# Kernel optimization log

Hardware: AMD Instinct MI355X
Metric: run time of the kernel (lower is better)

The kernel has to match this reference:

```python
import jax, jax.numpy as jnp
import numpy as np

B, HW, FEAT = 64, 196, 2048
EMB, HID, ATT, VOCAB, T = 512, 1024, 512, 10000, 20
STEPS = T - 1  # pack_padded_sequence uses lengths - 1


def setup_inputs() -> dict:
    key = jax.random.key(0)
    ks = jax.random.split(key, 16)
    rn = lambda k, s, sc=0.02: jax.random.normal(k, s, jnp.float32) * sc
    return {
        "features": jax.random.normal(ks[0], (B, HW, FEAT), jnp.float32),
        "captions": jax.random.randint(ks[1], (B, T), 0, VOCAB),
        "lengths": jnp.full((B,), T, jnp.int32),  # uniform lengths -> constant batch per step
        "E": rn(ks[2], (VOCAB, EMB)),
        "W_feat": rn(ks[3], (EMB, FEAT)), "b_feat": jnp.zeros((EMB,), jnp.float32),
        "W1": rn(ks[4], (ATT, EMB)), "b1": jnp.zeros((ATT,), jnp.float32),
        "W2": rn(ks[5], (ATT, HID)), "b2": jnp.zeros((ATT,), jnp.float32),
        "V": rn(ks[6], (1, ATT)), "bV": jnp.zeros((1,), jnp.float32),
        "W_hi": rn(ks[7], (HID, EMB)), "b_hi": jnp.zeros((HID,), jnp.float32),
        "W_ci": rn(ks[8], (HID, EMB)), "b_ci": jnp.zeros((HID,), jnp.float32),
        "W_ih": rn(ks[9], (4 * HID, 2 * EMB)), "b_ih": jnp.zeros((4 * HID,), jnp.float32),
        "W_hh": rn(ks[10], (4 * HID, HID)), "b_hh": jnp.zeros((4 * HID,), jnp.float32),
        "W_out": rn(ks[11], (VOCAB, HID)), "b_out": jnp.zeros((VOCAB,), jnp.float32),
    }


def reference(features, captions, lengths, E, W_feat, b_feat, W1, b1, W2, b2,
              V, bV, W_hi, b_hi, W_ci, b_ci, W_ih, b_ih, W_hh, b_hh, W_out, b_out):
    # features -> embed space: [B, HW, EMB]
    f = jnp.einsum('bhc,ec->bhe', features, W_feat) + b_feat
    fmean = f.mean(axis=1)                      # [B, EMB]
    hx0 = fmean @ W_hi.T + b_hi                 # [B, HID]
    cx0 = fmean @ W_ci.T + b_ci                 # [B, HID]
    fa = jnp.einsum('bhe,ae->bha', f, W1) + b1  # W1(features), [B, HW, ATT]

    emb = E[captions]                           # [B, T, EMB]
    xs = jnp.swapaxes(emb[:, :STEPS], 0, 1)     # [STEPS, B, EMB] teacher-forced inputs

    def step(carry, x):
        hx, cx = carry
        # Bahdanau attention
        ha = hx @ W2.T + b2                             # [B, ATT]
        score = jnp.tanh(fa + ha[:, None, :])           # [B, HW, ATT]
        logits = jnp.einsum('bha,oa->bho', score, V) + bV   # [B, HW, 1]
        w = jax.nn.softmax(logits, axis=1)              # softmax over HW
        ctx = jnp.sum(w * f, axis=1)                    # [B, EMB]
        # LSTMCell (PyTorch gate order: i, f, g, o)
        inp = jnp.concatenate([x, ctx], axis=1)         # [B, 2*EMB]
        gates = inp @ W_ih.T + b_ih + hx @ W_hh.T + b_hh
        i_g, f_g, g_g, o_g = jnp.split(gates, 4, axis=1)
        cx_n = jax.nn.sigmoid(f_g) * cx + jax.nn.sigmoid(i_g) * jnp.tanh(g_g)
        hx_n = jax.nn.sigmoid(o_g) * jnp.tanh(cx_n)
        out = hx_n @ W_out.T + b_out                    # dropout = identity (eval)
        return (hx_n, cx_n), out

    _, outs = jax.lax.scan(step, (hx0, cx0), xs)        # [STEPS, B, VOCAB]
    # torch.cat(outputs) over constant per-step batch == flatten time-major
    return outs.reshape(STEPS * B, VOCAB)
```

## Files before the change

### kernel.cpp

```cpp
#include <hip/hip_runtime.h>
#include <hip/hip_bf16.h>
#include <math.h>

#define BB 64
#define HW 196
#define FEAT 2048
#define EMB 512
#define HID 1024
#define ATT 512
#define VOCAB 10000
#define TT 20
#define STEPS 19

using bfrag = __attribute__((ext_vector_type(8))) short;
using f32x4 = __attribute__((ext_vector_type(4))) float;

__device__ __forceinline__ float sigmoid_fast(float x) { return 1.0f / (1.0f + __expf(-x)); }
__device__ __forceinline__ float tanh_fast(float x) {
    float e = __expf(2.0f * x);
    return 1.0f - 2.0f / (e + 1.0f);
}
__device__ __forceinline__ ushort f2bf_rne(float f) {
    unsigned u = __float_as_uint(f);
    unsigned r = (u + 0x7FFFu + ((u >> 16) & 1u)) >> 16;
    return (ushort)r;
}
__device__ __forceinline__ float bf2f(ushort h) {
    return __uint_as_float(((unsigned)h) << 16);
}

__global__ __launch_bounds__(256) void k_split(const float* __restrict__ x,
                                               ushort* __restrict__ hi,
                                               ushort* __restrict__ lo, int n)
{
    int i4 = (blockIdx.x * 256 + threadIdx.x) * 4;
    if (i4 >= n) return;
    float4 v = *(const float4*)(x + i4);
    float av[4] = {v.x, v.y, v.z, v.w};
    #pragma unroll
    for (int j = 0; j < 4; ++j) {
        ushort h = f2bf_rne(av[j]);
        hi[i4 + j] = h;
        lo[i4 + j] = f2bf_rne(av[j] - bf2f(h));
    }
}

template<bool ABF32, bool NFAST>
__global__ __launch_bounds__(256) void mfma_g(
    const float* __restrict__ A,
    const ushort* __restrict__ Ahi, const ushort* __restrict__ Alo,
    const ushort* __restrict__ Bhi, const ushort* __restrict__ Blo,
    const float* __restrict__ bias, float* __restrict__ C,
    ushort* __restrict__ Chi, ushort* __restrict__ Clo,
    int N, int K, int ldc, int NXB, int NMB)
{
    __shared__ __align__(16) ushort sAh[4][64][8];
    __shared__ __align__(16) ushort sAl[4][64][8];
    __shared__ __align__(16) ushort sBh[4][128][8];
    __shared__ __align__(16) ushort sBl[4][128][8];

    const int tid = threadIdx.x;

    const int nwg = NXB * NMB;
    const int q = nwg >> 3, r = nwg & 7;
    const int xcd = blockIdx.x & 7, sidx = blockIdx.x >> 3;
    const int wg = (xcd < r) ? (xcd * (q + 1) + sidx)
                             : (r * (q + 1) + (xcd - r) * q + sidx);
    int im, inb;
    if (NFAST) { inb = wg % NXB; im = wg / NXB; }
    else       { im = wg % NMB; inb = wg / NMB; }
    const int m0 = im * 64;
    const int n0 = inb * 128;

    const int lane = tid & 63;
    const int w = tid >> 6;
    const int mh = (w & 1) * 32;
    const int nh = (w >> 1) * 64;
    const int g = lane >> 4, l15 = lane & 15;

    f32x4 acc[2][4] = {};

    for (int k0 = 0; k0 < K; k0 += 32) {
        __syncthreads();
        if (ABF32) {
            int r_ = tid >> 2, g_ = tid & 3;
            const float* ap = A + (size_t)(m0 + r_) * K + k0 + g_ * 8;
            float av[8];
            *(float4*)(av)     = *(const float4*)(ap);
            *(float4*)(av + 4) = *(const float4*)(ap + 4);
            bfrag vh, vl;
            #pragma unroll
            for (int j = 0; j < 8; ++j) {
                ushort h = f2bf_rne(av[j]);
                vh[j] = (short)h;
                vl[j] = (short)f2bf_rne(av[j] - bf2f(h));
            }
            *(bfrag*)&sAh[g_][r_][0] = vh;
            *(bfrag*)&sAl[g_][r_][0] = vl;
        } else {
            #pragma unroll
            for (int i = 0; i < 2; ++i) {
                int c = tid + i * 256;
                int pl = c >> 8, idx2 = c & 255;
                int r_ = idx2 >> 2, g_ = idx2 & 3;
                const ushort* src = (pl ? Alo : Ahi) + (size_t)(m0 + r_) * K + k0 + g_ * 8;
                if (pl) *(bfrag*)&sAl[g_][r_][0] = *(const bfrag*)src;
                else    *(bfrag*)&sAh[g_][r_][0] = *(const bfrag*)src;
            }
        }
        #pragma unroll
        for (int i = 0; i < 4; ++i) {
            int c = tid + i * 256;
            int pl = c >> 9, idx2 = c & 511;
            int r_ = idx2 >> 2, g_ = idx2 & 3;
            int brow = min(n0 + r_, N - 1);
            const ushort* src = (pl ? Blo : Bhi) + (size_t)brow * K + k0 + g_ * 8;
            if (pl) *(bfrag*)&sBl[g_][r_][0] = *(const bfrag*)src;
            else    *(bfrag*)&sBh[g_][r_][0] = *(const bfrag*)src;
        }
        __syncthreads();

        bfrag ah[2], al[2], bh[4], bl[4];
        #pragma unroll
        for (int s = 0; s < 2; ++s) {
            ah[s] = *(const bfrag*)&sAh[g][mh + s * 16 + l15][0];
            al[s] = *(const bfrag*)&sAl[g][mh + s * 16 + l15][0];
        }
        #pragma unroll
        for (int u = 0; u < 4; ++u) {
            bh[u] = *(const bfrag*)&sBh[g][nh + u * 16 + l15][0];
            bl[u] = *(const bfrag*)&sBl[g][nh + u * 16 + l15][0];
        }
        #pragma unroll
        for (int s = 0; s < 2; ++s)
            #pragma unroll
            for (int u = 0; u < 4; ++u) {
                acc[s][u] = __builtin_amdgcn_mfma_f32_16x16x32_bf16(ah[s], bh[u], acc[s][u], 0, 0, 0);
                acc[s][u] = __builtin_amdgcn_mfma_f32_16x16x32_bf16(ah[s], bl[u], acc[s][u], 0, 0, 0);
                acc[s][u] = __builtin_amdgcn_mfma_f32_16x16x32_bf16(al[s], bh[u], acc[s][u], 0, 0, 0);
            }
    }

    #pragma unroll
    for (int s = 0; s < 2; ++s)
        #pragma unroll
        for (int u = 0; u < 4; ++u) {
            int col = n0 + nh + u * 16 + l15;
            if (col < N) {
                float bv = bias[col];
                #pragma unroll
                for (int rr = 0; rr < 4; ++rr) {
                    int row = m0 + mh + s * 16 + g * 4 + rr;
                    float v = acc[s][u][rr] + bv;
                    C[(size_t)row * ldc + col] = v;
                    if (Chi) {
                        ushort hh = f2bf_rne(v);
                        Chi[(size_t)row * ldc + col] = hh;
                        Clo[(size_t)row * ldc + col] = f2bf_rne(v - bf2f(hh));
                    }
                }
            }
        }
}

__global__ __launch_bounds__(256) void k_fmean(const float* __restrict__ f,
                                               float* __restrict__ fmean)
{
    int b = blockIdx.x, tid = threadIdx.x;
    for (int e = tid; e < EMB; e += 256) {
        const float* fb = f + (size_t)b * HW * EMB + e;
        float s = 0.f;
        for (int h = 0; h < HW; ++h) s += fb[(size_t)h * EMB];
        fmean[b * EMB + e] = s * (1.0f / HW);
    }
}

__global__ __launch_bounds__(256) void k_init(
    const float* __restrict__ fmean,
    const float* __restrict__ W_hi, const float* __restrict__ b_hi,
    const float* __restrict__ W_ci, const float* __restrict__ b_ci,
    float* __restrict__ hx, float* __restrict__ cx)
{
    int b = blockIdx.x, tid = threadIdx.x;
    __shared__ float fm[EMB];
    for (int i = tid; i < EMB; i += 256) fm[i] = fmean[b * EMB + i];
    __syncthreads();
    for (int u = tid; u < HID; u += 256) {
        const float4* w1 = (const float4*)(W_hi + (size_t)u * EMB);
        const float4* w2 = (const float4*)(W_ci + (size_t)u * EMB);
        float a1 = b_hi[u], a2 = b_ci[u];
        for (int k = 0; k < EMB / 4; ++k) {
            float4 y1 = w1[k], y2 = w2[k];
            float x0 = fm[4*k], x1 = fm[4*k+1], x2 = fm[4*k+2], x3 = fm[4*k+3];
            a1 += x0*y1.x + x1*y1.y + x2*y1.z + x3*y1.w;
            a2 += x0*y2.x + x1*y2.y + x2*y2.z + x3*y2.w;
        }
        hx[b * HID + u] = a1;
        cx[b * HID + u] = a2;
    }
}

__global__ __launch_bounds__(128) void k_embed_split(
    const int* __restrict__ cap, const float* __restrict__ E,
    ushort* __restrict__ xs_hi, ushort* __restrict__ xs_lo)
{
    int blk = blockIdx.x;
    int t = blk / BB, b = blk % BB;
    int c = cap[b * TT + t];
    float4 v = ((const float4*)(E + (size_t)c * EMB))[threadIdx.x];
    float av[4] = {v.x, v.y, v.z, v.w};
    ushort h[4], l[4];
    #pragma unroll
    for (int j = 0; j < 4; ++j) {
        h[j] = f2bf_rne(av[j]);
        l[j] = f2bf_rne(av[j] - bf2f(h[j]));
    }
    size_t base = ((size_t)t * BB + b) * EMB + threadIdx.x * 4;
    *(ushort4*)(xs_hi + base) = make_ushort4(h[0], h[1], h[2], h[3]);
    *(ushort4*)(xs_lo + base) = make_ushort4(l[0], l[1], l[2], l[3]);
}

__global__ __launch_bounds__(256) void k_ha(
    const float* __restrict__ hx, const float* __restrict__ W2,
    const float* __restrict__ b2, float* __restrict__ ha)
{
    __shared__ __align__(16) float hx_s[8][1028];
    __shared__ float part[256];
    const int tid = threadIdx.x;
    const int a0 = (blockIdx.x >> 3) * 16;
    const int b0 = (blockIdx.x & 7) * 8;

    for (int i = tid; i < 8 * 256; i += 256) {
        int r = i >> 8, c4 = i & 255;
        *(float4*)&hx_s[r][c4 * 4] = *(const float4*)(hx + (size_t)(b0 + r) * HID + c4 * 4);
    }
    __syncthreads();

    const int a_i = tid >> 4;
    const int b_i = (tid >> 1) & 7;
    const int half = tid & 1;
    const float4* wr = (const float4*)(W2 + (size_t)(a0 + a_i) * HID + half * 512);
    const float* xr = &hx_s[b_i][half * 512];
    float s = 0.f;
    #pragma unroll 8
    for (int i = 0; i < 128; ++i) {
        float4 w = wr[i];
        float4 x = *(const float4*)(xr + i * 4);
        s += w.x*x.x + w.y*x.y + w.z*x.z + w.w*x.w;
    }
    part[tid] = s;
    __syncthreads();
    if (!half)
        ha[(size_t)(b0 + b_i) * ATT + a0 + a_i] = part[tid] + part[tid + 1] + b2[a0 + a_i];
}

__global__ __launch_bounds__(1024) void k_att(
    const float* __restrict__ f, const float* __restrict__ fa,
    const float* __restrict__ ha, const float* __restrict__ V,
    ushort* __restrict__ ctx_hi, ushort* __restrict__ ctx_lo)
{
    __shared__ __align__(16) float smem[2048];
    const int b = blockIdx.x;
    const int tid = threadIdx.x;
    const int lane = tid & 63;
    const int wid = tid >> 6;

    float* ha_s = smem;
    float* V_s  = smem + 512;
    float* w_s  = smem + 1024;
    float* red  = smem + 1280;
    float* pc   = smem + 1536;

    if (tid < ATT) { ha_s[tid] = ha[b * ATT + tid]; V_s[tid] = V[tid]; }
    __syncthreads();

    for (int h = wid; h < HW; h += 16) {
        const float4* fr = (const float4*)(fa + ((size_t)b * HW + h) * ATT);
        float s = 0.f;
        #pragma unroll
        for (int q = 0; q < 2; ++q) {
            int i4 = q * 64 + lane;
            float4 fv = fr[i4];
            float4 hv = *(const float4*)&ha_s[i4 * 4];
            float4 vv = *(const float4*)&V_s[i4 * 4];
            s += tanh_fast(fv.x + hv.x) * vv.x + tanh_fast(fv.y + hv.y) * vv.y
               + tanh_fast(fv.z + hv.z) * vv.z + tanh_fast(fv.w + hv.w) * vv.w;
        }
        #pragma unroll
        for (int off = 32; off > 0; off >>= 1) s += __shfl_down(s, off);
        if (lane == 0) w_s[h] = s;
    }
    __syncthreads();

    float v = (tid < HW) ? w_s[tid] : -INFINITY;
    if (tid < 256) red[tid] = v;
    __syncthreads();
    for (int s2 = 128; s2 > 0; s2 >>= 1) {
        if (tid < s2) red[tid] = fmaxf(red[tid], red[tid + s2]);
        __syncthreads();
    }
    float mx = red[0];
    __syncthreads();
    float e = (tid < HW) ? __expf(v - mx) : 0.f;
    if (tid < 256) red[tid] = e;
    __syncthreads();
    for (int s2 = 128; s2 > 0; s2 >>= 1) {
        if (tid < s2) red[tid] += red[tid + s2];
        __syncthreads();
    }
    float inv = 1.0f / red[0];
    if (tid < HW) w_s[tid] = e * inv;
    __syncthreads();

    {
        int e0 = tid & 511, grp = tid >> 9;
        const float* fb = f + (size_t)b * HW * EMB + e0;
        float s = 0.f;
        int h0 = grp * 98;
        for (int h = h0; h < h0 + 98; ++h)
            s = fmaf(w_s[h], fb[(size_t)h * EMB], s);
        if (grp) pc[e0] = s;
        __syncthreads();
        if (!grp) {
            float c = s + pc[e0];
            ushort ch = f2bf_rne(c);
            ctx_hi[b * EMB + e0] = ch;
            ctx_lo[b * EMB + e0] = f2bf_rne(c - bf2f(ch));
        }
    }
}

__global__ __launch_bounds__(256) void k_gates_lstm(
    const ushort* __restrict__ xsh, const ushort* __restrict__ xsl,
    const ushort* __restrict__ cth, const ushort* __restrict__ ctl,
    const ushort* __restrict__ hxh, const ushort* __restrict__ hxl,
    const ushort* __restrict__ wihh, const ushort* __restrict__ wihl,
    const ushort* __restrict__ whhh, const ushort* __restrict__ whhl,
    const float* __restrict__ b_ih, const float* __restrict__ b_hh,
    float* __restrict__ hx, float* __restrict__ cx,
    ushort* __restrict__ nxh, ushort* __restrict__ nxl,
    float* __restrict__ hx_all_t,
    ushort* __restrict__ hxa_h, ushort* __restrict__ hxa_l)
{
    __shared__ float sg[64][16];
    const int tid = threadIdx.x, bk = blockIdx.x;
    const int lane = tid & 63, mt = tid >> 6;
    const int l15 = lane & 15, g = lane >> 4;
    const int arow = mt * 16 + l15;
    const int ncol = (l15 >> 2) * 1024 + bk * 4 + (l15 & 3);
    const int koff = g * 8;

    f32x4 acc0 = {}, acc1 = {};

    {
        const ushort* ah = xsh + (size_t)arow * 512 + koff;
        const ushort* al = xsl + (size_t)arow * 512 + koff;
        const ushort* bh = wihh + (size_t)ncol * 1024 + koff;
        const ushort* bl = wihl + (size_t)ncol * 1024 + koff;
        #pragma unroll 4
        for (int kk = 0; kk < 16; ++kk) {
            bfrag a_h = *(const bfrag*)(ah + kk * 32);
            bfrag a_l = *(const bfrag*)(al + kk * 32);
            bfrag b_h = *(const bfrag*)(bh + kk * 32);
            bfrag b_l = *(const bfrag*)(bl + kk * 32);
            acc0 = __builtin_amdgcn_mfma_f32_16x16x32_bf16(a_h, b_h, acc0, 0, 0, 0);
            acc1 = __builtin_amdgcn_mfma_f32_16x16x32_bf16(a_h, b_l, acc1, 0, 0, 0);
            acc1 = __builtin_amdgcn_mfma_f32_16x16x32_bf16(a_l, b_h, acc1, 0, 0, 0);
        }
    }
    {
        const ushort* ah = cth + (size_t)arow * 512 + koff;
        const ushort* al = ctl + (size_t)arow * 512 + koff;
        const ushort* bh = wihh + (size_t)ncol * 1024 + 512 + koff;
        const ushort* bl = wihl + (size_t)ncol * 1024 + 512 + koff;
        #pragma unroll 4
        for (int kk = 0; kk < 16; ++kk) {
            bfrag a_h = *(const bfrag*)(ah + kk * 32);
            bfrag a_l = *(const bfrag*)(al + kk * 32);
            bfrag b_h = *(const bfrag*)(bh + kk * 32);
            bfrag b_l = *(const bfrag*)(bl + kk * 32);
            acc0 = __builtin_amdgcn_mfma_f32_16x16x32_bf16(a_h, b_h, acc0, 0, 0, 0);
            acc1 = __builtin_amdgcn_mfma_f32_16x16x32_bf16(a_h, b_l, acc1, 0, 0, 0);
            acc1 = __builtin_amdgcn_mfma_f32_16x16x32_bf16(a_l, b_h, acc1, 0, 0, 0);
        }
    }
    {
        const ushort* ah = hxh + (size_t)arow * 1024 + koff;
        const ushort* al = hxl + (size_t)arow * 1024 + koff;
        const ushort* bh = whhh + (size_t)ncol * 1024 + koff;
        const ushort* bl = whhl + (size_t)ncol * 1024 + koff;
        #pragma unroll 4
        for (int kk = 0; kk < 32; ++kk) {
            bfrag a_h = *(const bfrag*)(ah + kk * 32);
            bfrag a_l = *(const bfrag*)(al + kk * 32);
            bfrag b_h = *(const bfrag*)(bh + kk * 32);
            bfrag b_l = *(const bfrag*)(bl + kk * 32);
            acc0 = __builtin_amdgcn_mfma_f32_16x16x32_bf16(a_h, b_h, acc0, 0, 0, 0);
            acc1 = __builtin_amdgcn_mfma_f32_16x16x32_bf16(a_h, b_l, acc1, 0, 0, 0);
            acc1 = __builtin_amdgcn_mfma_f32_16x16x32_bf16(a_l, b_h, acc1, 0, 0, 0);
        }
    }

    #pragma unroll
    for (int rr = 0; rr < 4; ++rr)
        sg[mt * 16 + g * 4 + rr][l15] = acc0[rr] + acc1[rr];
    __syncthreads();

    {
        int b = tid >> 2, uu = tid & 3;
        int u = bk * 4 + uu;
        float gi = sg[b][uu]      + b_ih[u]        + b_hh[u];
        float gf = sg[b][4 + uu]  + b_ih[1024 + u] + b_hh[1024 + u];
        float gg = sg[b][8 + uu]  + b_ih[2048 + u] + b_hh[2048 + u];
        float go = sg[b][12 + uu] + b_ih[3072 + u] + b_hh[3072 + u];
        int idx = b * 1024 + u;
        float c = sigmoid_fast(gf) * cx[idx] + sigmoid_fast(gi) * tanh_fast(gg);
        float h = sigmoid_fast(go) * tanh_fast(c);
        cx[idx] = c;
        hx[idx] = h;
        hx_all_t[idx] = h;
        ushort hh = f2bf_rne(h);
        ushort hl = f2bf_rne(h - bf2f(hh));
        nxh[idx] = hh; nxl[idx] = hl;
        hxa_h[idx] = hh; hxa_l[idx] = hl;
    }
}

extern "C" void kernel_launch(void* const* d_in, const int* in_sizes, int n_in,
                              void* d_out, int out_size, void* d_ws, size_t ws_size,
                              hipStream_t stream) {
    const float* features = (const float*)d_in[0];
    const int*   captions = (const int*)d_in[1];
    const float* E      = (const float*)d_in[3];
    const float* W_feat = (const float*)d_in[4];
    const float* b_feat = (const float*)d_in[5];
    const float* W1     = (const float*)d_in[6];
    const float* b1     = (const float*)d_in[7];
    const float* W2     = (const float*)d_in[8];
    const float* b2     = (const float*)d_in[9];
    const float* V      = (const float*)d_in[10];
    const float* W_hi   = (const float*)d_in[12];
    const float* b_hi   = (const float*)d_in[13];
    const float* W_ci   = (const float*)d_in[14];
    const float* b_ci   = (const float*)d_in[15];
    const float* W_ih   = (const float*)d_in[16];
    const float* b_ih   = (const float*)d_in[17];
    const float* W_hh   = (const float*)d_in[18];
    const float* b_hh   = (const float*)d_in[19];
    const float* W_out  = (const float*)d_in[20];
    const float* b_out  = (const float*)d_in[21];
    float* out = (float*)d_out;

    float* ws = (float*)d_ws;
    float* f_buf   = ws;
    float* fa_buf  = f_buf + 6422528;
    float* fmean   = fa_buf + 6422528;
    float* hx      = fmean + 32768;
    float* cx      = hx + 65536;
    float* hx_all  = cx + 65536;
    float* ha      = hx_all + 1310720;
    ushort* p = (ushort*)(ha + 32768);
    ushort* f_hi     = p;            p += 6422528;
    ushort* f_lo     = p;            p += 6422528;
    ushort* wfeat_hi = p;            p += 1048576;
    ushort* wfeat_lo = p;            p += 1048576;
    ushort* w1_hi    = p;            p += 262144;
    ushort* w1_lo    = p;            p += 262144;
    ushort* wih_hi   = p;            p += 4194304;
    ushort* wih_lo   = p;            p += 4194304;
    ushort* whh_hi   = p;            p += 4194304;
    ushort* whh_lo   = p;            p += 4194304;
    ushort* xs_hi    = p;            p += 622592;
    ushort* xs_lo    = p;            p += 622592;
    ushort* ctx_hi   = p;            p += 32768;
    ushort* ctx_lo   = p;            p += 32768;
    ushort* hxp      = p;            p += 262144;
    ushort* hxa_hi   = p;            p += 1310720;
    ushort* hxa_lo   = p;            p += 1310720;
    ushort* wout_hi = (ushort*)f_buf;
    ushort* wout_lo = wout_hi + 10240000;

    k_split<<<1048576 / 4 / 256, 256, 0, stream>>>(W_feat, wfeat_hi, wfeat_lo, 1048576);
    k_split<<<262144 / 4 / 256, 256, 0, stream>>>(W1, w1_hi, w1_lo, 262144);
    k_split<<<4194304 / 4 / 256, 256, 0, stream>>>(W_ih, wih_hi, wih_lo, 4194304);
    k_split<<<4194304 / 4 / 256, 256, 0, stream>>>(W_hh, whh_hi, whh_lo, 4194304);
    mfma_g<true, true><<<784, 256, 0, stream>>>(
        features, nullptr, nullptr, wfeat_hi, wfeat_lo, b_feat,
        f_buf, f_hi, f_lo, 512, 2048, 512, 4, 196);
    mfma_g<false, true><<<784, 256, 0, stream>>>(
        nullptr, f_hi, f_lo, w1_hi, w1_lo, b1,
        fa_buf, nullptr, nullptr, 512, 512, 512, 4, 196);
    k_fmean<<<BB, 256, 0, stream>>>(f_buf, fmean);
    k_init<<<BB, 256, 0, stream>>>(fmean, W_hi, b_hi, W_ci, b_ci, hx, cx);
    k_split<<<65536 / 4 / 256, 256, 0, stream>>>(hx, hxp, hxp + 65536, 65536);
    k_embed_split<<<STEPS * BB, 128, 0, stream>>>(captions, E, xs_hi, xs_lo);

    for (int t = 0; t < STEPS; ++t) {
        ushort* hx_rd = hxp + (size_t)(t & 1) * 131072;
        ushort* hx_wr = hxp + (size_t)((t + 1) & 1) * 131072;
        k_ha<<<256, 256, 0, stream>>>(hx, W2, b2, ha);
        k_att<<<BB, 1024, 0, stream>>>(f_buf, fa_buf, ha, V, ctx_hi, ctx_lo);
        k_gates_lstm<<<256, 256, 0, stream>>>(
            xs_hi + (size_t)t * BB * EMB, xs_lo + (size_t)t * BB * EMB,
            ctx_hi, ctx_lo, hx_rd, hx_rd + 65536,
            wih_hi, wih_lo, whh_hi, whh_lo, b_ih, b_hh,
            hx, cx, hx_wr, hx_wr + 65536,
            hx_all + (size_t)t * BB * HID,
            hxa_hi + (size_t)t * BB * HID, hxa_lo + (size_t)t * BB * HID);
    }

    k_split<<<10240000 / 4 / 256, 256, 0, stream>>>(W_out, wout_hi, wout_lo, 10240000);
    mfma_g<false, false><<<1501, 256, 0, stream>>>(
        nullptr, hxa_hi, hxa_lo, wout_hi, wout_lo, b_out,
        out, nullptr, nullptr, VOCAB, HID, VOCAB, 79, 19);
}
```

Baseline: 1.887 ms.

## Swizzle LDS tiles, drop bf16 split buffers, split LSTM gate K across waves

The GEMM kernel now always reads fp32 A and splits it into hi/lo bf16 in-register, which removes the f_hi/f_lo and hxa_hi/hxa_lo intermediate buffers and their global writes. Shared-memory tiles use an XOR swizzle on the 16-byte chunk index to reduce LDS bank conflicts. The LSTM gate kernel doubles its threads so that the input-projection and recurrent-projection halves run on separate waves, with the partial sums combined through shared memory. The trade-off is re-splitting A inside every GEMM tile, which adds conversion ALU work and more fp32 read bandwidth.

Result: faster. 1.798 ms (-4.7%).

```diff
diff --git a/kernel.cpp b/kernel.cpp
--- a/kernel.cpp
+++ b/kernel.cpp
@@ -28,6 +28,7 @@
 __device__ __forceinline__ float bf2f(ushort h) {
     return __uint_as_float(((unsigned)h) << 16);
 }
+__device__ __forceinline__ int sw_idx(int row, int g) { return row * 4 + (g ^ (row & 3)); }
 
 __global__ __launch_bounds__(256) void k_split(const float* __restrict__ x,
                                                ushort* __restrict__ hi,
@@ -45,19 +46,17 @@
     }
 }
 
-template<bool ABF32, bool NFAST>
+template<bool NFAST>
 __global__ __launch_bounds__(256) void mfma_g(
     const float* __restrict__ A,
-    const ushort* __restrict__ Ahi, const ushort* __restrict__ Alo,
     const ushort* __restrict__ Bhi, const ushort* __restrict__ Blo,
     const float* __restrict__ bias, float* __restrict__ C,
-    ushort* __restrict__ Chi, ushort* __restrict__ Clo,
     int N, int K, int ldc, int NXB, int NMB)
 {
-    __shared__ __align__(16) ushort sAh[4][64][8];
-    __shared__ __align__(16) ushort sAl[4][64][8];
-    __shared__ __align__(16) ushort sBh[4][128][8];
-    __shared__ __align__(16) ushort sBl[4][128][8];
+    __shared__ __align__(16) ushort sAh[256 * 8];
+    __shared__ __align__(16) ushort sAl[256 * 8];
+    __shared__ __align__(16) ushort sBh[512 * 8];
+    __shared__ __align__(16) ushort sBl[512 * 8];
 
     const int tid = threadIdx.x;
 
@@ -82,7 +81,7 @@
 
     for (int k0 = 0; k0 < K; k0 += 32) {
         __syncthreads();
-        if (ABF32) {
+        {
             int r_ = tid >> 2, g_ = tid & 3;
             const float* ap = A + (size_t)(m0 + r_) * K + k0 + g_ * 8;
             float av[8];
@@ -95,18 +94,9 @@
                 vh[j] = (short)h;
                 vl[j] = (short)f2bf_rne(av[j] - bf2f(h));
             }
-            *(bfrag*)&sAh[g_][r_][0] = vh;
-            *(bfrag*)&sAl[g_][r_][0] = vl;
-        } else {
-            #pragma unroll
-            for (int i = 0; i < 2; ++i) {
-                int c = tid + i * 256;
-                int pl = c >> 8, idx2 = c & 255;
-                int r_ = idx2 >> 2, g_ = idx2 & 3;
-                const ushort* src = (pl ? Alo : Ahi) + (size_t)(m0 + r_) * K + k0 + g_ * 8;
-                if (pl) *(bfrag*)&sAl[g_][r_][0] = *(const bfrag*)src;
-                else    *(bfrag*)&sAh[g_][r_][0] = *(const bfrag*)src;
-            }
+            int c = sw_idx(r_, g_) * 8;
+            *(bfrag*)&sAh[c] = vh;
+            *(bfrag*)&sAl[c] = vl;
         }
         #pragma unroll
         for (int i = 0; i < 4; ++i) {
@@ -115,21 +105,24 @@
             int r_ = idx2 >> 2, g_ = idx2 & 3;
             int brow = min(n0 + r_, N - 1);
             const ushort* src = (pl ? Blo : Bhi) + (size_t)brow * K + k0 + g_ * 8;
-            if (pl) *(bfrag*)&sBl[g_][r_][0] = *(const bfrag*)src;
-            else    *(bfrag*)&sBh[g_][r_][0] = *(const bfrag*)src;
+            int cc = sw_idx(r_, g_) * 8;
+            if (pl) *(bfrag*)&sBl[cc] = *(const bfrag*)src;
+            else    *(bfrag*)&sBh[cc] = *(const bfrag*)src;
         }
         __syncthreads();
 
         bfrag ah[2], al[2], bh[4], bl[4];
         #pragma unroll
         for (int s = 0; s < 2; ++s) {
-            ah[s] = *(const bfrag*)&sAh[g][mh + s * 16 + l15][0];
-            al[s] = *(const bfrag*)&sAl[g][mh + s * 16 + l15][0];
+            int c = sw_idx(mh + s * 16 + l15, g) * 8;
+            ah[s] = *(const bfrag*)&sAh[c];
+            al[s] = *(const bfrag*)&sAl[c];
         }
         #pragma unroll
         for (int u = 0; u < 4; ++u) {
-            bh[u] = *(const bfrag*)&sBh[g][nh + u * 16 + l15][0];
-            bl[u] = *(const bfrag*)&sBl[g][nh + u * 16 + l15][0];
+            int c = sw_idx(nh + u * 16 + l15, g) * 8;
+            bh[u] = *(const bfrag*)&sBh[c];
+            bl[u] = *(const bfrag*)&sBl[c];
         }
         #pragma unroll
         for (int s = 0; s < 2; ++s)
@@ -151,13 +144,7 @@
                 #pragma unroll
                 for (int rr = 0; rr < 4; ++rr) {
                     int row = m0 + mh + s * 16 + g * 4 + rr;
-                    float v = acc[s][u][rr] + bv;
-                    C[(size_t)row * ldc + col] = v;
-                    if (Chi) {
-                        ushort hh = f2bf_rne(v);
-                        Chi[(size_t)row * ldc + col] = hh;
-                        Clo[(size_t)row * ldc + col] = f2bf_rne(v - bf2f(hh));
-                    }
+                    C[(size_t)row * ldc + col] = acc[s][u][rr] + bv;
                 }
             }
         }
@@ -330,7 +317,7 @@
     }
 }
 
-__global__ __launch_bounds__(256) void k_gates_lstm(
+__global__ __launch_bounds__(512) void k_gates_lstm(
     const ushort* __restrict__ xsh, const ushort* __restrict__ xsl,
     const ushort* __restrict__ cth, const ushort* __restrict__ ctl,
     const ushort* __restrict__ hxh, const ushort* __restrict__ hxl,
@@ -339,12 +326,12 @@
     const float* __restrict__ b_ih, const float* __restrict__ b_hh,
     float* __restrict__ hx, float* __restrict__ cx,
     ushort* __restrict__ nxh, ushort* __restrict__ nxl,
-    float* __restrict__ hx_all_t,
-    ushort* __restrict__ hxa_h, ushort* __restrict__ hxa_l)
-{
-    __shared__ float sg[64][16];
+    float* __restrict__ hx_all_t)
+{
+    __shared__ float sg[2][64][16];
     const int tid = threadIdx.x, bk = blockIdx.x;
-    const int lane = tid & 63, mt = tid >> 6;
+    const int lane = tid & 63, wid = tid >> 6;
+    const int mt = wid & 3, kh = wid >> 2;
     const int l15 = lane & 15, g = lane >> 4;
     const int arow = mt * 16 + l15;
     const int ncol = (l15 >> 2) * 1024 + bk * 4 + (l15 & 3);
@@ -352,39 +339,40 @@
 
     f32x4 acc0 = {}, acc1 = {};
 
-    {
-        const ushort* ah = xsh + (size_t)arow * 512 + koff;
-        const ushort* al = xsl + (size_t)arow * 512 + koff;
-        const ushort* bh = wihh + (size_t)ncol * 1024 + koff;
-        const ushort* bl = wihl + (size_t)ncol * 1024 + koff;
-        #pragma unroll 4
-        for (int kk = 0; kk < 16; ++kk) {
-            bfrag a_h = *(const bfrag*)(ah + kk * 32);
-            bfrag a_l = *(const bfrag*)(al + kk * 32);
-            bfrag b_h = *(const bfrag*)(bh + kk * 32);
-            bfrag b_l = *(const bfrag*)(bl + kk * 32);
-            acc0 = __builtin_amdgcn_mfma_f32_16x16x32_bf16(a_h, b_h, acc0, 0, 0, 0);
-            acc1 = __builtin_amdgcn_mfma_f32_16x16x32_bf16(a_h, b_l, acc1, 0, 0, 0);
-            acc1 = __builtin_amdgcn_mfma_f32_16x16x32_bf16(a_l, b_h, acc1, 0, 0, 0);
-        }
-    }
-    {
-        const ushort* ah = cth + (size_t)arow * 512 + koff;
-        const ushort* al = ctl + (size_t)arow * 512 + koff;
-        const ushort* bh = wihh + (size_t)ncol * 1024 + 512 + koff;
-        const ushort* bl = wihl + (size_t)ncol * 1024 + 512 + koff;
-        #pragma unroll 4
-        for (int kk = 0; kk < 16; ++kk) {
-            bfrag a_h = *(const bfrag*)(ah + kk * 32);
-            bfrag a_l = *(const bfrag*)(al + kk * 32);
-            bfrag b_h = *(const bfrag*)(bh + kk * 32);
-            bfrag b_l = *(const bfrag*)(bl + kk * 32);
-            acc0 = __builtin_amdgcn_mfma_f32_16x16x32_bf16(a_h, b_h, acc0, 0, 0, 0);
-            acc1 = __builtin_amdgcn_mfma_f32_16x16x32_bf16(a_h, b_l, acc1, 0, 0, 0);
-            acc1 = __builtin_amdgcn_mfma_f32_16x16x32_bf16(a_l, b_h, acc1, 0, 0, 0);
-        }
-    }
-    {
+    if (kh == 0) {
+        {
+            const ushort* ah = xsh + (size_t)arow * 512 + koff;
+            const ushort* al = xsl + (size_t)arow * 512 + koff;
+            const ushort* bh = wihh + (size_t)ncol * 1024 + koff;
+            const ushort* bl = wihl + (size_t)ncol * 1024 + koff;
+            #pragma unroll 4
+            for (int kk = 0; kk < 16; ++kk) {
+                bfrag a_h = *(const bfrag*)(ah + kk * 32);
+                bfrag a_l = *(const bfrag*)(al + kk * 32);
+                bfrag b_h = *(const bfrag*)(bh + kk * 32);
+                bfrag b_l = *(const bfrag*)(bl + kk * 32);
+                acc0 = __builtin_amdgcn_mfma_f32_16x16x32_bf16(a_h, b_h, acc0, 0, 0, 0);
+                acc1 = __builtin_amdgcn_mfma_f32_16x16x32_bf16(a_h, b_l, acc1, 0, 0, 0);
+                acc1 = __builtin_amdgcn_mfma_f32_16x16x32_bf16(a_l, b_h, acc1, 0, 0, 0);
+            }
+        }
+        {
+            const ushort* ah = cth + (size_t)arow * 512 + koff;
+            const ushort* al = ctl + (size_t)arow * 512 + koff;
+            const ushort* bh = wihh + (size_t)ncol * 1024 + 512 + koff;
+            const ushort* bl = wihl + (size_t)ncol * 1024 + 512 + koff;
+            #pragma unroll 4
+            for (int kk = 0; kk < 16; ++kk) {
+                bfrag a_h = *(const bfrag*)(ah + kk * 32);
+                bfrag a_l = *(const bfrag*)(al + kk * 32);
+                bfrag b_h = *(const bfrag*)(bh + kk * 32);
+                bfrag b_l = *(const bfrag*)(bl + kk * 32);
+                acc0 = __builtin_amdgcn_mfma_f32_16x16x32_bf16(a_h, b_h, acc0, 0, 0, 0);
+                acc1 = __builtin_amdgcn_mfma_f32_16x16x32_bf16(a_h, b_l, acc1, 0, 0, 0);
+                acc1 = __builtin_amdgcn_mfma_f32_16x16x32_bf16(a_l, b_h, acc1, 0, 0, 0);
+            }
+        }
+    } else {
         const ushort* ah = hxh + (size_t)arow * 1024 + koff;
         const ushort* al = hxl + (size_t)arow * 1024 + koff;
         const ushort* bh = whhh + (size_t)ncol * 1024 + koff;
@@ -403,16 +391,16 @@
 
     #pragma unroll
     for (int rr = 0; rr < 4; ++rr)
-        sg[mt * 16 + g * 4 + rr][l15] = acc0[rr] + acc1[rr];
-    __syncthreads();
-
-    {
+        sg[kh][mt * 16 + g * 4 + rr][l15] = acc0[rr] + acc1[rr];
+    __syncthreads();
+
+    if (tid < 256) {
         int b = tid >> 2, uu = tid & 3;
         int u = bk * 4 + uu;
-        float gi = sg[b][uu]      + b_ih[u]        + b_hh[u];
-        float gf = sg[b][4 + uu]  + b_ih[1024 + u] + b_hh[1024 + u];
-        float gg = sg[b][8 + uu]  + b_ih[2048 + u] + b_hh[2048 + u];
-        float go = sg[b][12 + uu] + b_ih[3072 + u] + b_hh[3072 + u];
+        float gi = sg[0][b][uu]      + sg[1][b][uu]      + b_ih[u]        + b_hh[u];
+        float gf = sg[0][b][4 + uu]  + sg[1][b][4 + uu]  + b_ih[1024 + u] + b_hh[1024 + u];
+        float gg = sg[0][b][8 + uu]  + sg[1][b][8 + uu]  + b_ih[2048 + u] + b_hh[2048 + u];
+        float go = sg[0][b][12 + uu] + sg[1][b][12 + uu] + b_ih[3072 + u] + b_hh[3072 + u];
         int idx = b * 1024 + u;
         float c = sigmoid_fast(gf) * cx[idx] + sigmoid_fast(gi) * tanh_fast(gg);
         float h = sigmoid_fast(go) * tanh_fast(c);
@@ -420,9 +408,8 @@
         hx[idx] = h;
         hx_all_t[idx] = h;
         ushort hh = f2bf_rne(h);
-        ushort hl = f2bf_rne(h - bf2f(hh));
-        nxh[idx] = hh; nxl[idx] = hl;
-        hxa_h[idx] = hh; hxa_l[idx] = hl;
+        nxh[idx] = hh;
+        nxl[idx] = f2bf_rne(h - bf2f(hh));
     }
 }
 
@@ -460,8 +447,6 @@
     float* hx_all  = cx + 65536;
     float* ha      = hx_all + 1310720;
     ushort* p = (ushort*)(ha + 32768);
-    ushort* f_hi     = p;            p += 6422528;
-    ushort* f_lo     = p;            p += 6422528;
     ushort* wfeat_hi = p;            p += 1048576;
     ushort* wfeat_lo = p;            p += 1048576;
     ushort* w1_hi    = p;            p += 262144;
@@ -475,8 +460,6 @@
     ushort* ctx_hi   = p;            p += 32768;
     ushort* ctx_lo   = p;            p += 32768;
     ushort* hxp      = p;            p += 262144;
-    ushort* hxa_hi   = p;            p += 1310720;
-    ushort* hxa_lo   = p;            p += 1310720;
     ushort* wout_hi = (ushort*)f_buf;
     ushort* wout_lo = wout_hi + 10240000;
 
@@ -484,12 +467,10 @@
     k_split<<<262144 / 4 / 256, 256, 0, stream>>>(W1, w1_hi, w1_lo, 262144);
     k_split<<<4194304 / 4 / 256, 256, 0, stream>>>(W_ih, wih_hi, wih_lo, 4194304);
     k_split<<<4194304 / 4 / 256, 256, 0, stream>>>(W_hh, whh_hi, whh_lo, 4194304);
-    mfma_g<true, true><<<784, 256, 0, stream>>>(
-        features, nullptr, nullptr, wfeat_hi, wfeat_lo, b_feat,
-        f_buf, f_hi, f_lo, 512, 2048, 512, 4, 196);
-    mfma_g<false, true><<<784, 256, 0, stream>>>(
-        nullptr, f_hi, f_lo, w1_hi, w1_lo, b1,
-        fa_buf, nullptr, nullptr, 512, 512, 512, 4, 196);
+    mfma_g<true><<<784, 256, 0, stream>>>(
+        features, wfeat_hi, wfeat_lo, b_feat, f_buf, 512, 2048, 512, 4, 196);
+    mfma_g<true><<<784, 256, 0, stream>>>(
+        f_buf, w1_hi, w1_lo, b1, fa_buf, 512, 512, 512, 4, 196);
     k_fmean<<<BB, 256, 0, stream>>>(f_buf, fmean);
     k_init<<<BB, 256, 0, stream>>>(fmean, W_hi, b_hi, W_ci, b_ci, hx, cx);
     k_split<<<65536 / 4 / 256, 256, 0, stream>>>(hx, hxp, hxp + 65536, 65536);
@@ -500,17 +481,15 @@
         ushort* hx_wr = hxp + (size_t)((t + 1) & 1) * 131072;
         k_ha<<<256, 256, 0, stream>>>(hx, W2, b2, ha);
         k_att<<<BB, 1024, 0, stream>>>(f_buf, fa_buf, ha, V, ctx_hi, ctx_lo);
-        k_gates_lstm<<<256, 256, 0, stream>>>(
+        k_gates_lstm<<<256, 512, 0, stream>>>(
             xs_hi + (size_t)t * BB * EMB, xs_lo + (size_t)t * BB * EMB,
             ctx_hi, ctx_lo, hx_rd, hx_rd + 65536,
             wih_hi, wih_lo, whh_hi, whh_lo, b_ih, b_hh,
             hx, cx, hx_wr, hx_wr + 65536,
-            hx_all + (size_t)t * BB * HID,
-            hxa_hi + (size_t)t * BB * HID, hxa_lo + (size_t)t * BB * HID);
+            hx_all + (size_t)t * BB * HID);
     }
 
     k_split<<<10240000 / 4 / 256, 256, 0, stream>>>(W_out, wout_hi, wout_lo, 10240000);
-    mfma_g<false, false><<<1501, 256, 0, stream>>>(
-        nullptr, hxa_hi, hxa_lo, wout_hi, wout_lo, b_out,
-        out, nullptr, nullptr, VOCAB, HID, VOCAB, 79, 19);
-}
+    mfma_g<false><<<1501, 256, 0, stream>>>(
+        hx_all, wout_hi, wout_lo, b_out, out, VOCAB, HID, VOCAB, 79, 19);
+}
```
